# Optimization experiments

Measured on AMD Instinct MI355X. Metric: run time of the kernel, lower is better.

Reference implementation:

```python
import jax, jax.numpy as jnp
import numpy as np

D_MODEL = 512
NUM_HEADS = 8
HEAD_DIM = D_MODEL // NUM_HEADS
NEG_INF = -1e9


def setup_inputs() -> dict:
    key = jax.random.key(0)
    ks = jax.random.split(key, 12)
    B, S = 4, 2048
    std = 1.0 / np.sqrt(D_MODEL)
    inp = {
        "query": jax.random.normal(ks[0], (B, S, D_MODEL), jnp.float32),
        "key": jax.random.normal(ks[1], (B, S, D_MODEL), jnp.float32),
        "value": jax.random.normal(ks[2], (B, S, D_MODEL), jnp.float32),
        "mask": jax.random.randint(ks[3], (B, 1, S, S), 0, 2, jnp.int32),
        "Wq": jax.random.normal(ks[4], (D_MODEL, D_MODEL), jnp.float32) * std,
        "bq": jnp.zeros((D_MODEL,), jnp.float32),
        "Wk": jax.random.normal(ks[5], (D_MODEL, D_MODEL), jnp.float32) * std,
        "bk": jnp.zeros((D_MODEL,), jnp.float32),
        "Wv": jax.random.normal(ks[6], (D_MODEL, D_MODEL), jnp.float32) * std,
        "bv": jnp.zeros((D_MODEL,), jnp.float32),
        "Wo": jax.random.normal(ks[7], (D_MODEL, D_MODEL), jnp.float32) * std,
        "bo": jnp.zeros((D_MODEL,), jnp.float32),
    }
    return inp


def _split_heads(x):
    B, S, _ = x.shape
    return x.reshape(B, S, NUM_HEADS, HEAD_DIM).transpose(0, 2, 1, 3)  # [B,H,S,Dh]


def reference(query, key, value, mask, Wq, bq, Wk, bk, Wv, bv, Wo, bo):
    B, S, _ = query.shape
    q = _split_heads(query @ Wq + bq)
    k = _split_heads(key @ Wk + bk)
    v = _split_heads(value @ Wv + bv)
    # scores: [B,H,S,S]
    scores = jnp.einsum("bhqd,bhkd->bhqk", q, k) / jnp.sqrt(jnp.float32(HEAD_DIM))
    scores = jnp.where(mask == 0, jnp.float32(NEG_INF), scores)
    attn = jax.nn.softmax(scores, axis=-1)  # dropout p=0 -> identity
    out = jnp.einsum("bhqk,bhkd->bhqd", attn, v)
    out = out.transpose(0, 2, 1, 3).reshape(B, S, D_MODEL)
    return out @ Wo + bo
```

## Files before the change

kernel.cpp:

```cpp
#include <hip/hip_runtime.h>
#include <hip/hip_bf16.h>

typedef unsigned short u16;
typedef __attribute__((ext_vector_type(4))) float f32x4;
typedef __attribute__((ext_vector_type(16))) float f32x16;
typedef __attribute__((ext_vector_type(8))) short s16x8;
typedef __attribute__((ext_vector_type(4))) unsigned short u16x4;

__device__ __forceinline__ u16 f2bf(float f) {
    union { float f; unsigned u; } v; v.f = f;
    unsigned r = v.u + 0x7fffu + ((v.u >> 16) & 1u);
    return (u16)(r >> 16);
}
__device__ __forceinline__ u16 f2bfh(float f) {
    __hip_bfloat16 h = __float2bfloat16(f);
    return *reinterpret_cast<u16*>(&h);
}
__device__ __forceinline__ float bf2f(u16 h) {
    union { unsigned u; float f; } v; v.u = ((unsigned)h) << 16;
    return v.f;
}
__device__ __forceinline__ float fexp2(float x) {
#if __has_builtin(__builtin_amdgcn_exp2f)
    return __builtin_amdgcn_exp2f(x);
#else
    return exp2f(x);
#endif
}
__device__ __forceinline__ void gload16(const void* g, void* lds_uniform) {
    __builtin_amdgcn_global_load_lds(
        (const __attribute__((address_space(1))) void*)g,
        (__attribute__((address_space(3))) void*)lds_uniform, 16, 0, 0);
}
__device__ __forceinline__ f32x4 mfma16(s16x8 a, s16x8 b, f32x4 c) {
    return __builtin_amdgcn_mfma_f32_16x16x32_bf16(a, b, c, 0, 0, 0);
}
__device__ __forceinline__ f32x16 mfma32(s16x8 a, s16x8 b, f32x16 c) {
    return __builtin_amdgcn_mfma_f32_32x32x16_bf16(a, b, c, 0, 0, 0);
}

__global__ void prep(const float4* __restrict__ q, const float4* __restrict__ k,
                     const float4* __restrict__ v, u16x4* __restrict__ qkv,
                     const float* __restrict__ Wq, const float* __restrict__ Wk,
                     const float* __restrict__ Wv, const float* __restrict__ Wo,
                     u16* __restrict__ WqT, u16* __restrict__ WkT,
                     u16* __restrict__ WvT, u16* __restrict__ WoT,
                     const int* __restrict__ mask, unsigned* __restrict__ bits) {
    __shared__ float tile[32][33];
    const int bid = blockIdx.x, tid = threadIdx.x;
    if (bid < 12288) {
        int i = bid * 256 + tid;
        int sel = i >> 20, j = i & 0xFFFFF;
        const float4* in = (sel == 0) ? q : (sel == 1) ? k : v;
        float4 f = in[j];
        u16x4 o;
        o[0] = f2bf(f.x); o[1] = f2bf(f.y); o[2] = f2bf(f.z); o[3] = f2bf(f.w);
        qkv[i] = o;
    } else if (bid < 13312) {
        int idx = bid - 12288;
        int bz = idx >> 8, rem = idx & 255, by = rem >> 4, bx = rem & 15;
        const float* W; u16* T;
        switch (bz) {
            case 0: W = Wq; T = WqT; break;
            case 1: W = Wk; T = WkT; break;
            case 2: W = Wv; T = WvT; break;
            default: W = Wo; T = WoT; break;
        }
        const int tx = tid & 31, ty = tid >> 5;
        const int k0 = by * 32, n0 = bx * 32;
#pragma unroll
        for (int r = 0; r < 32; r += 8) tile[ty + r][tx] = W[(k0 + ty + r) * 512 + n0 + tx];
        __syncthreads();
#pragma unroll
        for (int r = 0; r < 32; r += 8) T[(n0 + ty + r) * 512 + k0 + tx] = f2bf(tile[tx][ty + r]);
    } else {
        int i = (bid - 13312) * 256 + tid;
        int m = mask[i];
        unsigned long long bal = __ballot(m != 0);
        if ((tid & 63) == 0) {
            uint2 w2; w2.x = (unsigned)bal; w2.y = (unsigned)(bal >> 32);
            *(uint2*)&bits[i >> 5] = w2;
        }
    }
}

template <int BM, int BIAS_ROW, int OUT_F32, int XSMALL>
__global__ __launch_bounds__(256, 4) void gemm_bt(
    const u16* __restrict__ A, const u16* __restrict__ Bt0, const u16* __restrict__ Bt1,
    const float* __restrict__ bias0, const float* __restrict__ bias1,
    void* __restrict__ Cout, int M, int N, int K, int ysplit,
    float scale0, float scale1) {
    constexpr int MR = BM / 32;
    const int bidl = blockIdx.x + blockIdx.y * gridDim.x;
    const int xcd = bidl & 7, slot = bidl >> 3;
    const int big = slot >> 3, small = slot & 7;
    int bx, by;
    if (XSMALL) { bx = small; by = xcd * ((int)gridDim.y >> 3) + big; }
    else        { by = small; bx = xcd * ((int)gridDim.x >> 3) + big; }
    const u16* Bt = (by < ysplit) ? Bt0 : Bt1;
    const float* bias = (by < ysplit) ? bias0 : bias1;
    const float scale = (by < ysplit) ? scale0 : scale1;
    __shared__ u16 As[BM * 64];
    __shared__ u16 Bs[64 * 64];
    const int t = threadIdx.x, l = t & 63, w = t >> 6;
    const int lr = l & 15, lg = l >> 4;
    const int m0 = by * BM, n0 = bx * 64;
    const int wr = w >> 1, wc = w & 1;
    f32x4 acc[MR][2] = {};
    const int tr = t >> 3, tc8 = (t & 7) * 8;

    for (int kk = 0; kk < K; kk += 64) {
        __syncthreads();
#pragma unroll
        for (int i = 0; i < MR; ++i)
            gload16(A + (m0 + i * 32 + tr) * K + kk + tc8, As + i * 2048 + w * 512);
#pragma unroll
        for (int i = 0; i < 2; ++i)
            gload16(Bt + (n0 + i * 32 + tr) * K + kk + tc8, Bs + i * 2048 + w * 512);
        __syncthreads();
        s16x8 af[MR][2], bfr[2][2];
#pragma unroll
        for (int m = 0; m < MR; ++m)
#pragma unroll
            for (int kh = 0; kh < 2; ++kh)
                af[m][kh] = *(const s16x8*)&As[(wr * (BM / 2) + m * 16 + lr) * 64 + kh * 32 + lg * 8];
#pragma unroll
        for (int n = 0; n < 2; ++n)
#pragma unroll
            for (int kh = 0; kh < 2; ++kh)
                bfr[n][kh] = *(const s16x8*)&Bs[(wc * 32 + n * 16 + lr) * 64 + kh * 32 + lg * 8];
#pragma unroll
        for (int m = 0; m < MR; ++m)
#pragma unroll
            for (int n = 0; n < 2; ++n)
#pragma unroll
                for (int kh = 0; kh < 2; ++kh)
                    acc[m][n] = mfma16(af[m][kh], bfr[n][kh], acc[m][n]);
    }

#pragma unroll
    for (int n = 0; n < 2; ++n) {
        const int cg = n0 + wc * 32 + n * 16 + lr;
        const float bcol = BIAS_ROW ? 0.f : bias[cg];
#pragma unroll
        for (int m = 0; m < MR; ++m) {
            const int rbase = m0 + wr * (BM / 2) + m * 16 + lg * 4;
#pragma unroll
            for (int j = 0; j < 4; ++j) {
                const int rg = rbase + j;
                float val = (acc[m][n][j] + (BIAS_ROW ? bias[rg] : bcol)) * scale;
                if (OUT_F32) ((float*)Cout)[(size_t)rg * N + cg] = val;
                else         ((u16*)Cout)[(size_t)rg * N + cg] = f2bf(val);
            }
        }
    }
}

__global__ __launch_bounds__(256, 4) void attn_fwd(
    const u16* __restrict__ Qp, const u16* __restrict__ Kp,
    const u16* __restrict__ Vt, const unsigned* __restrict__ mbits,
    u16* __restrict__ ppo, float* __restrict__ lws) {
    constexpr int S = 2048;
    const int bid = blockIdx.x;
    const int xcd = bid & 7, slot = bid >> 3;
    const int qt = slot & 15;
    const int combo = xcd * 8 + (slot >> 4);
    const int bh = combo & 31, z = combo >> 5;
    const int kbase = z << 10;
    const int b = bh >> 3, h = bh & 7;
    const int t = threadIdx.x, l = t & 63, w = t >> 6;
    const int lq = l & 31, hi = l >> 5;
    const int hi8 = hi * 8, hi4 = hi * 4;

    __shared__ u16 Ks[2][64 * 64];
    __shared__ u16 Vs[2][64 * 64];

    const int q0w = qt * 128 + w * 32;
    const int bS = b * S;

    s16x8 qf[4];
#pragma unroll
    for (int ds = 0; ds < 4; ++ds)
        qf[ds] = *(const s16x8*)&Qp[(bS + q0w + lq) * 512 + h * 64 + ds * 16 + hi8];

    f32x16 po[2];
#pragma unroll
    for (int r = 0; r < 16; ++r) { po[0][r] = 0.f; po[1][r] = 0.f; }
    float lrun = 0.f;

    const int kc0 = t, kc1 = 256 + t;
    const int krow0 = kc0 >> 3, kcol0 = ((kc0 & 7) ^ (krow0 & 7)) * 8;
    const int krow1 = kc1 >> 3, kcol1 = ((kc1 & 7) ^ (krow1 & 7)) * 8;

#define STAGE(nb, kt0)                                                              \
    do {                                                                            \
        gload16(&Kp[(bS + (kt0) + krow0) * 512 + h * 64 + kcol0], &Ks[nb][w * 512]);\
        gload16(&Kp[(bS + (kt0) + krow1) * 512 + h * 64 + kcol1], &Ks[nb][2048 + w * 512]);\
        gload16(&Vt[(h * 64 + krow0) * (4 * S) + bS + (kt0) + kcol0], &Vs[nb][w * 512]);\
        gload16(&Vt[(h * 64 + krow1) * (4 * S) + bS + (kt0) + kcol1], &Vs[nb][2048 + w * 512]);\
    } while (0)

    const int mrow = (bS + q0w + lq) * 64 + (kbase >> 5);
    STAGE(0, kbase);
    uint2 mwv = *(const uint2*)&mbits[mrow];
    uint2 mwn = mwv;

    for (int it = 0; it < 16; ++it) {
        const int cur = it & 1;
        __syncthreads();
        if (it + 1 < 16) {
            STAGE(cur ^ 1, kbase + (it + 1) * 64);
            mwn = *(const uint2*)&mbits[mrow + ((it + 1) << 1)];
        }
        const u16* Kc = Ks[cur];
        const u16* Vc = Vs[cur];

        s16x8 bq[4];
#pragma unroll
        for (int kt_t = 0; kt_t < 2; ++kt_t) {
            f32x16 sc;
#pragma unroll
            for (int r = 0; r < 16; ++r) sc[r] = 0.f;
            __builtin_amdgcn_s_setprio(1);
#pragma unroll
            for (int ds = 0; ds < 4; ++ds) {
                const int row = kt_t * 32 + lq;
                const int byte = (row * 128 + ds * 32 + hi * 16) ^ ((row & 7) << 4);
                s16x8 ka = *(const s16x8*)((const char*)Kc + byte);
                sc = mfma32(ka, qf[ds], sc);
            }
            __builtin_amdgcn_s_setprio(0);

            const unsigned w32s = (kt_t ? mwv.y : mwv.x) >> hi4;
            float p[16];
            float ps = 0.f;
#pragma unroll
            for (int r = 0; r < 16; ++r) {
                const unsigned bmask = 1u << ((r & 3) + 8 * (r >> 2));
                const float e = fexp2(sc[r]);
                p[r] = (w32s & bmask) ? e : 0.f;
                ps += p[r];
            }
            lrun += ps;

            unsigned pk[8];
#pragma unroll
            for (int i = 0; i < 8; ++i) {
                unsigned v;
                asm("v_cvt_pk_bf16_f32 %0, %1, %2"
                    : "=v"(v) : "v"(p[2 * i]), "v"(p[2 * i + 1]));
                pk[i] = v;
            }
            asm("v_permlane32_swap_b32 %0, %1" : "+v"(pk[0]), "+v"(pk[2]));
            asm("v_permlane32_swap_b32 %0, %1" : "+v"(pk[1]), "+v"(pk[3]));
            asm("v_permlane32_swap_b32 %0, %1" : "+v"(pk[4]), "+v"(pk[6]));
            asm("v_permlane32_swap_b32 %0, %1" : "+v"(pk[5]), "+v"(pk[7]));
            union BQ { unsigned u[4]; s16x8 v; } b0, b1;
            b0.u[0] = pk[0]; b0.u[1] = pk[1]; b0.u[2] = pk[2]; b0.u[3] = pk[3];
            b1.u[0] = pk[4]; b1.u[1] = pk[5]; b1.u[2] = pk[6]; b1.u[3] = pk[7];
            bq[kt_t * 2]     = b0.v;
            bq[kt_t * 2 + 1] = b1.v;
        }

        __builtin_amdgcn_s_setprio(1);
#pragma unroll
        for (int dt = 0; dt < 2; ++dt)
#pragma unroll
            for (int ks = 0; ks < 4; ++ks) {
                const int row = dt * 32 + lq;
                const int byte = (row * 128 + ks * 32 + hi * 16) ^ ((row & 7) << 4);
                s16x8 va = *(const s16x8*)((const char*)Vc + byte);
                po[dt] = mfma32(va, bq[ks], po[dt]);
            }
        __builtin_amdgcn_s_setprio(0);

        mwv = mwn;
    }
#undef STAGE

    lrun += __shfl_xor(lrun, 32);
    const float inv = 1.f / lrun;
    u16* pp = ppo + (size_t)z * 4194304;
    const int orow = (bS + q0w + lq) * 512 + h * 64;
#pragma unroll
    for (int dt = 0; dt < 2; ++dt)
#pragma unroll
        for (int r = 0; r < 16; r += 2) {
            const int d = dt * 32 + (r & 3) + 8 * (r >> 2) + hi4;
            const unsigned lo = f2bfh(po[dt][r] * inv);
            const unsigned hh = f2bfh(po[dt][r + 1] * inv);
            *(unsigned*)&pp[orow + d] = lo | (hh << 16);
        }
    if (hi == 0) lws[z * 65536 + bh * 2048 + q0w + lq] = lrun;
}

__global__ __launch_bounds__(256) void combine(const u16* __restrict__ po,
                                               const float* __restrict__ lw,
                                               u16* __restrict__ AO) {
    const int i = (blockIdx.x * 256 + threadIdx.x) * 8;
    const int row = i >> 9, col = i & 511;
    const int lidx = ((row >> 11) * 8 + (col >> 6)) * 2048 + (row & 2047);
    const float la = lw[lidx], lb = lw[65536 + lidx];
    const float wa = la / (la + lb), wb = 1.f - wa;
    s16x8 a = *(const s16x8*)&po[i];
    s16x8 c = *(const s16x8*)&po[4194304 + i];
    s16x8 o;
#pragma unroll
    for (int j = 0; j < 8; ++j)
        o[j] = (short)f2bfh(bf2f((u16)a[j]) * wa + bf2f((u16)c[j]) * wb);
    *(s16x8*)&AO[i] = o;
}

extern "C" void kernel_launch(void* const* d_in, const int* in_sizes, int n_in,
                              void* d_out, int out_size, void* d_ws, size_t ws_size,
                              hipStream_t stream) {
    (void)in_sizes; (void)n_in; (void)out_size; (void)ws_size;
    const float* query = (const float*)d_in[0];
    const float* key   = (const float*)d_in[1];
    const float* value = (const float*)d_in[2];
    const int*   mask  = (const int*)d_in[3];
    const float* Wq = (const float*)d_in[4];
    const float* bq = (const float*)d_in[5];
    const float* Wk = (const float*)d_in[6];
    const float* bk = (const float*)d_in[7];
    const float* Wv = (const float*)d_in[8];
    const float* bv = (const float*)d_in[9];
    const float* Wo = (const float*)d_in[10];
    const float* bo = (const float*)d_in[11];

    char* ws = (char*)d_ws;
    const size_t MB = 1ull << 20;
    u16* qb  = (u16*)(ws);
    u16* vb  = (u16*)(ws + 16 * MB);
    u16* WqT = (u16*)(ws + 24 * MB);
    u16* WkT = (u16*)(ws + 24 * MB + 512 * 1024);
    u16* WvT = (u16*)(ws + 25 * MB);
    u16* WoT = (u16*)(ws + 25 * MB + 512 * 1024);
    unsigned* mb = (unsigned*)(ws + 26 * MB);
    u16* Qp = (u16*)(ws + 28 * MB);
    u16* Vt = (u16*)(ws + 44 * MB);
    u16* AO = (u16*)(ws + 52 * MB);
    u16* ppo = (u16*)(ws);
    float* lws = (float*)(ws + 17 * MB);

    prep<<<78848, 256, 0, stream>>>((const float4*)query, (const float4*)key,
                                    (const float4*)value, (u16x4*)qb,
                                    Wq, Wk, Wv, Wo, WqT, WkT, WvT, WoT, mask, mb);

    gemm_bt<128, 0, 0, 1><<<dim3(8, 128), 256, 0, stream>>>(
        qb, WqT, WkT, bq, bk, Qp, 16384, 512, 512, 64, 0.18033688f, 1.0f);
    gemm_bt<64, 1, 0, 0><<<dim3(128, 8), 256, 0, stream>>>(
        WvT, vb, vb, bv, bv, Vt, 512, 8192, 512, 999, 1.0f, 1.0f);

    attn_fwd<<<1024, 256, 0, stream>>>(Qp, Qp + 8192 * 512, Vt, mb, ppo, lws);
    combine<<<2048, 256, 0, stream>>>(ppo, lws, AO);

    gemm_bt<64, 0, 1, 1><<<dim3(8, 128), 256, 0, stream>>>(
        AO, WoT, WoT, bo, bo, (float*)d_out, 8192, 512, 512, 999, 1.0f, 1.0f);
}
```

Before: 137.0 us.

## Load K and V fragments directly from global memory, dropping LDS staging

The attention kernel no longer double-buffers K and V tiles through shared memory with async global-to-LDS loads and block barriers. Each wave now reads its MFMA operands straight from global memory (relying on L2/L1 cache), and the mask word is loaded each iteration without prefetch. This removes the __syncthreads and LDS traffic and frees shared memory for occupancy. In exchange, the four waves in a block, which share the same K/V tile, now fetch it redundantly, and without prefetch the global load latency is exposed.

```diff
diff --git a/kernel.cpp b/kernel.cpp
--- a/kernel.cpp
+++ b/kernel.cpp
@@ -172,9 +172,6 @@
     const int lq = l & 31, hi = l >> 5;
     const int hi8 = hi * 8, hi4 = hi * 4;
 
-    __shared__ u16 Ks[2][64 * 64];
-    __shared__ u16 Vs[2][64 * 64];
-
     const int q0w = qt * 128 + w * 32;
     const int bS = b * S;
 
@@ -188,32 +185,13 @@
     for (int r = 0; r < 16; ++r) { po[0][r] = 0.f; po[1][r] = 0.f; }
     float lrun = 0.f;
 
-    const int kc0 = t, kc1 = 256 + t;
-    const int krow0 = kc0 >> 3, kcol0 = ((kc0 & 7) ^ (krow0 & 7)) * 8;
-    const int krow1 = kc1 >> 3, kcol1 = ((kc1 & 7) ^ (krow1 & 7)) * 8;
-
-#define STAGE(nb, kt0)                                                              \
-    do {                                                                            \
-        gload16(&Kp[(bS + (kt0) + krow0) * 512 + h * 64 + kcol0], &Ks[nb][w * 512]);\
-        gload16(&Kp[(bS + (kt0) + krow1) * 512 + h * 64 + kcol1], &Ks[nb][2048 + w * 512]);\
-        gload16(&Vt[(h * 64 + krow0) * (4 * S) + bS + (kt0) + kcol0], &Vs[nb][w * 512]);\
-        gload16(&Vt[(h * 64 + krow1) * (4 * S) + bS + (kt0) + kcol1], &Vs[nb][2048 + w * 512]);\
-    } while (0)
-
+    const u16* Kbase = Kp + (size_t)(bS + kbase + lq) * 512 + h * 64 + hi8;
+    const u16* Vbase = Vt + (size_t)(h * 64 + lq) * 8192 + bS + kbase + hi8;
     const int mrow = (bS + q0w + lq) * 64 + (kbase >> 5);
-    STAGE(0, kbase);
-    uint2 mwv = *(const uint2*)&mbits[mrow];
-    uint2 mwn = mwv;
 
     for (int it = 0; it < 16; ++it) {
-        const int cur = it & 1;
-        __syncthreads();
-        if (it + 1 < 16) {
-            STAGE(cur ^ 1, kbase + (it + 1) * 64);
-            mwn = *(const uint2*)&mbits[mrow + ((it + 1) << 1)];
-        }
-        const u16* Kc = Ks[cur];
-        const u16* Vc = Vs[cur];
+        const uint2 mwv = *(const uint2*)&mbits[mrow + (it << 1)];
+        const int ktb = it * 64;
 
         s16x8 bq[4];
 #pragma unroll
@@ -224,9 +202,7 @@
             __builtin_amdgcn_s_setprio(1);
 #pragma unroll
             for (int ds = 0; ds < 4; ++ds) {
-                const int row = kt_t * 32 + lq;
-                const int byte = (row * 128 + ds * 32 + hi * 16) ^ ((row & 7) << 4);
-                s16x8 ka = *(const s16x8*)((const char*)Kc + byte);
+                s16x8 ka = *(const s16x8*)&Kbase[(size_t)(ktb + kt_t * 32) * 512 + ds * 16];
                 sc = mfma32(ka, qf[ds], sc);
             }
             __builtin_amdgcn_s_setprio(0);
@@ -267,16 +243,11 @@
         for (int dt = 0; dt < 2; ++dt)
 #pragma unroll
             for (int ks = 0; ks < 4; ++ks) {
-                const int row = dt * 32 + lq;
-                const int byte = (row * 128 + ks * 32 + hi * 16) ^ ((row & 7) << 4);
-                s16x8 va = *(const s16x8*)((const char*)Vc + byte);
+                s16x8 va = *(const s16x8*)&Vbase[(size_t)(dt * 32) * 8192 + ktb + ks * 16];
                 po[dt] = mfma32(va, bq[ks], po[dt]);
             }
         __builtin_amdgcn_s_setprio(0);
-
-        mwv = mwn;
     }
-#undef STAGE
 
     lrun += __shfl_xor(lrun, 32);
     const float inv = 1.f / lrun;
```

Result: slower. 213.1 us (+55.6%).
